# Kernel tuning notes

Measured on AMD Instinct MI355X. Metric: run time of the kernel, lower is better.

Reference implementation:

```python
import jax, jax.numpy as jnp
import numpy as np

B, LMAX, H, D = 128, 256, 16, 64
NEG_INF = -1e9  # finite mask value to keep padded softmax rows NaN-free


def _lengths():
    # deterministic varlen mix: 64 seqs of 128 tokens, 64 of 256 -> total 24576
    lens = np.array([128] * 64 + [256] * 64, dtype=np.int64)
    rng = np.random.default_rng(0)
    rng.shuffle(lens)
    return lens


def setup_inputs() -> dict:
    key = jax.random.key(0)
    lens = _lengths()
    cu = np.zeros(B + 1, dtype=np.int64)
    cu[1:] = np.cumsum(lens)
    T = int(cu[-1])  # 24576 packed tokens

    kq, kk, kv = jax.random.split(key, 3)
    q = jax.random.normal(kq, (T, H, D), dtype=jnp.float32)
    k = jax.random.normal(kk, (T, H, D), dtype=jnp.float32)
    v = jax.random.normal(kv, (T, H, D), dtype=jnp.float32)

    pos = np.arange(LMAX)[None, :]                      # [1, LMAX]
    mask = pos < lens[:, None]                          # [B, LMAX] valid-token mask
    gather_idx = np.where(mask, cu[:-1, None] + pos, 0).astype(np.int32)

    # packed token t -> flat padded index b*LMAX + (t - cu[b])
    b_of = np.repeat(np.arange(B), lens)
    inv_idx = (b_of * LMAX + (np.arange(T) - cu[b_of])).astype(np.int32)

    return {
        "q": q, "k": k, "v": v,
        "cu_seqlens_q": jnp.asarray(cu, dtype=jnp.int32),
        "cu_seqlens_k": jnp.asarray(cu, dtype=jnp.int32),
        "gather_idx": jnp.asarray(gather_idx),
        "mask": jnp.asarray(mask),
        "inv_idx": jnp.asarray(inv_idx),
        "max_seqlen_q": LMAX,
        "max_seqlen_k": LMAX,
    }


def reference(q, k, v, cu_seqlens_q, cu_seqlens_k, gather_idx, mask, inv_idx,
              max_seqlen_q, max_seqlen_k):
    # Pad packed [T,H,D] -> [B,L,H,D]; padded slots point at token 0 but are masked out.
    qp = q[gather_idx]  # [B, L, H, D]
    kp = k[gather_idx]
    vp = v[gather_idx]
    scale = 1.0 / jnp.sqrt(jnp.asarray(q.shape[-1], q.dtype))
    scores = jnp.einsum("bqhd,bkhd->bhqk", qp, kp) * scale  # [B, H, L, L]
    scores = jnp.where(mask[:, None, None, :], scores, NEG_INF)
    w = jax.nn.softmax(scores, axis=-1)
    out_p = jnp.einsum("bhqk,bkhd->bqhd", w, vp)            # [B, L, H, D]
    # Unpad back to packed layout [T, H, D]
    return out_p.reshape(-1, q.shape[1], q.shape[2])[inv_idx]
```

## Files before the change

kernel.cpp:

```cpp
#include <hip/hip_runtime.h>
#include <hip/hip_bf16.h>


using bf16x8 = __attribute__((ext_vector_type(8))) short;
using u16x8  = __attribute__((ext_vector_type(8))) unsigned short;
using u32x4  = __attribute__((ext_vector_type(4))) unsigned;
using f32x16 = __attribute__((ext_vector_type(16))) float;

#define MFMA32(a, b, c) __builtin_amdgcn_mfma_f32_32x32x16_bf16((a), (b), (c), 0, 0, 0)

constexpr int H  = 16;
constexpr int D  = 64;
constexpr int RS = H * D;
constexpr int NITEMS = 128 * 16;
constexpr float QSCALE = 0.125f * 1.44269504088896f;
constexpr float THR    = 11.5f;

__device__ inline unsigned short bfbits(float x) {
  return __builtin_bit_cast(unsigned short, __float2bfloat16(x));
}
__device__ inline float bff(unsigned short u) {
  unsigned v = ((unsigned)u) << 16;
  return __builtin_bit_cast(float, v);
}
__device__ inline unsigned pack2(float x, float y) {
  return (unsigned)bfbits(x) | ((unsigned)bfbits(y) << 16);
}

__global__ __launch_bounds__(512, 2)
void fa_persist13_kernel(const float* __restrict__ qg, const float* __restrict__ kg,
                         const float* __restrict__ vg, const int* __restrict__ cu,
                         float* __restrict__ outg, int* __restrict__ ctr) {
  __shared__ unsigned short kp4[4][64 * 64];
  __shared__ unsigned short vt4[4][64 * 64];
  __shared__ float lsc[8 * 32];
  __shared__ int item_s2[2];

  const int tid = (int)threadIdx.x, lane = tid & 63, w = tid >> 6;
  const int hi = lane >> 5, qj = lane & 31;
  const bool hib = (hi != 0);

  const int m7   = qj & 7;
  const int boff = (hi ^ m7) << 3;
  const int KA0  = qj * 64 + boff;
  const int KA1  = (32 + qj) * 64 + boff;

  const int k_key = tid >> 3, kd0 = (tid & 7) * 8;
  const int kidx  = k_key * 64 + ((((kd0 >> 3)) ^ (k_key & 7)) << 3);
  const int v_d = tid & 63, vk0 = (tid >> 6) * 8;
  const int vidx  = v_d * 64 + ((((vk0 >> 3)) ^ (v_d & 7)) << 3);

  if (tid == 0) item_s2[0] = atomicAdd(ctr, 1);
  int parity = 0;

  for (;;) {
    __syncthreads();
    const int item = item_s2[parity];
    if (item >= NITEMS) break;

    const int b = item >> 4, h = item & 15;
    const int t0 = cu[b];
    const int L  = cu[b + 1] - t0;
    const bool pair = (L == 128);
    if (pair && h >= 8) {
      if (tid == 0) item_s2[parity ^ 1] = atomicAdd(ctr, 1);
      parity ^= 1;
      continue;
    }

    const int myh    = pair ? ((w < 4) ? h : h + 8) : h;
    const int q_roff = pair ? (w & 3) * 32 : w * 32;
    const int hD  = h * D;
    const int h2D = (h + 8) * D;
    const int t_v1 = pair ? 0  : 64;  const int ho_v1 = pair ? h2D : hD;
    const int t_v2 = pair ? 64 : 128; const int ho_v2 = hD;
    const int t_v3 = pair ? 64 : 192; const int ho_v3 = pair ? h2D : hD;

    bf16x8 qh[4], ql[4];
    {
      const float* qrow = qg + (size_t)(t0 + q_roff + qj) * RS + (size_t)(myh * D);
#pragma unroll
      for (int ks = 0; ks < 4; ++ks) {
        const int d0 = ks * 16 + hi * 8;
        const float4 f0 = *reinterpret_cast<const float4*>(qrow + d0);
        const float4 f1 = *reinterpret_cast<const float4*>(qrow + d0 + 4);
        const float f[8] = {f0.x, f0.y, f0.z, f0.w, f1.x, f1.y, f1.z, f1.w};
#pragma unroll
        for (int j = 0; j < 8; ++j) {
          const float x = f[j] * QSCALE;
          const unsigned short hs = bfbits(x);
          qh[ks][j] = (short)hs;
          ql[ks][j] = (short)bfbits(x - bff(hs));
        }
      }
    }

    f32x16 acc0, acc1;
#pragma unroll
    for (int r = 0; r < 16; ++r) { acc0[r] = 0.f; acc1[r] = 0.f; }
    float m = -1e30f, lsum = 0.f;

    auto load_t = [&](float* kf, float* vf, int tokoff, int ho) {
      const float* kr = kg + (size_t)(t0 + tokoff + k_key) * RS + (size_t)(ho + kd0);
      const float4 f0 = *reinterpret_cast<const float4*>(kr);
      const float4 f1 = *reinterpret_cast<const float4*>(kr + 4);
      kf[0] = f0.x; kf[1] = f0.y; kf[2] = f0.z; kf[3] = f0.w;
      kf[4] = f1.x; kf[5] = f1.y; kf[6] = f1.z; kf[7] = f1.w;
      const float* vp = vg + (size_t)(t0 + tokoff + vk0) * RS + (size_t)(ho + v_d);
#pragma unroll
      for (int i = 0; i < 8; ++i) vf[i] = vp[(size_t)i * RS];
    };
    auto cvt_write = [&](const float* kf, const float* vf, int buf) {
      u16x8 kh8, v8;
#pragma unroll
      for (int i = 0; i < 8; ++i) {
        kh8[i] = bfbits(kf[i]);
        v8[i]  = bfbits(vf[i]);
      }
      *reinterpret_cast<u16x8*>(&kp4[buf][kidx]) = kh8;
      *reinterpret_cast<u16x8*>(&vt4[buf][vidx]) = v8;
    };

    auto mix4 = [&](unsigned a0, unsigned a1, unsigned a2, unsigned a3) -> u32x4 {
      const unsigned t02 = hib ? a0 : a2;
      const unsigned t13 = hib ? a1 : a3;
      const unsigned c02 = (unsigned)__shfl_xor((int)t02, 32);
      const unsigned c13 = (unsigned)__shfl_xor((int)t13, 32);
      u32x4 r;
      r[0] = hib ? c02 : a0;
      r[1] = hib ? c13 : a1;
      r[2] = hib ? a2 : c02;
      r[3] = hib ? a3 : c13;
      return r;
    };
    auto build_pa = [&](const float* x) -> bf16x8 {
      return __builtin_bit_cast(bf16x8,
          mix4(pack2(x[0], x[1]), pack2(x[2], x[3]),
               pack2(x[4], x[5]), pack2(x[6], x[7])));
    };

    auto compute = [&](const unsigned short* KH, const unsigned short* VT) {
      f32x16 sc0, sc1;
#pragma unroll
      for (int r = 0; r < 16; ++r) { sc0[r] = 0.f; sc1[r] = 0.f; }
#pragma unroll
      for (int ks = 0; ks < 4; ++ks) {
        const bf16x8 k0 = *reinterpret_cast<const bf16x8*>(&KH[KA0 ^ (ks << 4)]);
        sc0 = MFMA32(k0, qh[ks], sc0);
        sc0 = MFMA32(k0, ql[ks], sc0);
      }
#pragma unroll
      for (int ks = 0; ks < 4; ++ks) {
        const bf16x8 k1 = *reinterpret_cast<const bf16x8*>(&KH[KA1 ^ (ks << 4)]);
        sc1 = MFMA32(k1, qh[ks], sc1);
        sc1 = MFMA32(k1, ql[ks], sc1);
      }

      float mx[8];
#pragma unroll
      for (int i = 0; i < 8; ++i) mx[i] = fmaxf(sc0[i], sc0[i + 8]);
#pragma unroll
      for (int i = 0; i < 8; ++i) mx[i] = fmaxf(mx[i], fmaxf(sc1[i], sc1[i + 8]));
#pragma unroll
      for (int i = 0; i < 4; ++i) mx[i] = fmaxf(mx[i], mx[i + 4]);
      float tmax = fmaxf(fmaxf(mx[0], mx[1]), fmaxf(mx[2], mx[3]));
      tmax = fmaxf(tmax, __shfl_xor(tmax, 32));
      if (!__all(tmax <= m + THR)) {
        const float newm = fmaxf(m, tmax);
        const float corr = exp2f(m - newm);
        m = newm;
        lsum *= corr;
        if (hi == 0) lsc[w * 32 + qj] = corr;
        __builtin_amdgcn_wave_barrier();
#pragma unroll
        for (int r = 0; r < 16; ++r) {
          const float c = lsc[w * 32 + ((r & 3) + 8 * (r >> 2) + 4 * hi)];
          acc0[r] *= c; acc1[r] *= c;
        }
      }
      float s0 = 0.f, s1 = 0.f, s2 = 0.f, s3 = 0.f;
#pragma unroll
      for (int r = 0; r < 16; r += 4) {
        sc0[r]     = exp2f(sc0[r]     - m); s0 += sc0[r];
        sc0[r + 1] = exp2f(sc0[r + 1] - m); s1 += sc0[r + 1];
        sc0[r + 2] = exp2f(sc0[r + 2] - m); s2 += sc0[r + 2];
        sc0[r + 3] = exp2f(sc0[r + 3] - m); s3 += sc0[r + 3];
      }
#pragma unroll
      for (int r = 0; r < 16; r += 4) {
        sc1[r]     = exp2f(sc1[r]     - m); s0 += sc1[r];
        sc1[r + 1] = exp2f(sc1[r + 1] - m); s1 += sc1[r + 1];
        sc1[r + 2] = exp2f(sc1[r + 2] - m); s2 += sc1[r + 2];
        sc1[r + 3] = exp2f(sc1[r + 3] - m); s3 += sc1[r + 3];
      }
      lsum += (s0 + s1) + (s2 + s3);

#pragma unroll
      for (int ks2 = 0; ks2 < 4; ++ks2) {
        float px[8];
#pragma unroll
        for (int i = 0; i < 8; ++i)
          px[i] = (ks2 & 2) ? sc1[(ks2 & 1) * 8 + i] : sc0[(ks2 & 1) * 8 + i];
        const bf16x8 pah = build_pa(px);
        const bf16x8 v0 = *reinterpret_cast<const bf16x8*>(&VT[KA0 ^ (ks2 << 4)]);
        const bf16x8 v1 = *reinterpret_cast<const bf16x8*>(&VT[KA1 ^ (ks2 << 4)]);
        acc0 = MFMA32(pah, v0, acc0);
        acc1 = MFMA32(pah, v1, acc1);
      }
    };

#define LGKM_BARRIER()                                    \
    asm volatile("s_waitcnt lgkmcnt(0)" ::: "memory");    \
    __builtin_amdgcn_s_barrier();                         \
    asm volatile("" ::: "memory")

    float kfA[8], vfA[8], kfB[8], vfB[8];
    load_t(kfA, vfA, 0, hD);
    load_t(kfB, vfB, t_v1, ho_v1);
    cvt_write(kfA, vfA, 0);
    cvt_write(kfB, vfB, 1);
    LGKM_BARRIER();

    if (pair) {
      load_t(kfA, vfA, t_v2, ho_v2);
      load_t(kfB, vfB, t_v3, ho_v3);
      const int c1 = (w < 4) ? 0 : 1;
      compute(kp4[c1], vt4[c1]);
      cvt_write(kfA, vfA, 2);
      cvt_write(kfB, vfB, 3);
      LGKM_BARRIER();
      if (tid == 0) item_s2[parity ^ 1] = atomicAdd(ctr, 1);
      const int c2 = (w < 4) ? 2 : 3;
      compute(kp4[c2], vt4[c2]);
    } else {
      load_t(kfA, vfA, t_v2, ho_v2);
      compute(kp4[0], vt4[0]);
      cvt_write(kfA, vfA, 2);
      load_t(kfB, vfB, t_v3, ho_v3);
      compute(kp4[1], vt4[1]);
      cvt_write(kfB, vfB, 3);
      LGKM_BARRIER();
      if (tid == 0) item_s2[parity ^ 1] = atomicAdd(ctr, 1);
      compute(kp4[2], vt4[2]);
      compute(kp4[3], vt4[3]);
    }

    lsum += __shfl_xor(lsum, 32);
    if (hi == 0) lsc[w * 32 + qj] = 1.0f / lsum;
    __builtin_amdgcn_wave_barrier();
#pragma unroll
    for (int r = 0; r < 16; ++r) {
      const int row = (r & 3) + 8 * (r >> 2) + 4 * hi;
      const float li = lsc[w * 32 + row];
      float* op = outg + (size_t)(t0 + q_roff + row) * RS + (size_t)(myh * D) + qj;
      op[0]  = acc0[r] * li;
      op[32] = acc1[r] * li;
    }
    parity ^= 1;
  }
#undef LGKM_BARRIER
}

extern "C" void kernel_launch(void* const* d_in, const int* in_sizes, int n_in,
                              void* d_out, int out_size, void* d_ws, size_t ws_size,
                              hipStream_t stream) {
  (void)in_sizes; (void)n_in; (void)ws_size; (void)out_size;
  const float* q  = (const float*)d_in[0];
  const float* k  = (const float*)d_in[1];
  const float* v  = (const float*)d_in[2];
  const int*   cu = (const int*)d_in[3];
  float* out = (float*)d_out;
  int*   ctr = (int*)d_ws;

  hipMemsetAsync(ctr, 0, sizeof(int), stream);
  fa_persist13_kernel<<<dim3(512), dim3(512), 0, stream>>>(q, k, v, cu, out, ctr);
}
```

Before: 102.9 us.

## Prefetch next work item's first K/V tiles during current item's compute

Moves the atomic fetch of the next work item ahead of the barrier, then issues global loads for the next item's first two K/V tiles before the final compute phase of the current item. The aim is to hide the global-memory latency at the start of each persistent-loop iteration behind MFMA work. The cost is more live registers across the compute phase, which could cause spills or hurt the two-blocks-per-CU occupancy. The atomicAdd now sits before the lgkmcnt wait so its LDS write becomes visible after the barrier.

```diff
diff --git a/kernel.cpp b/kernel.cpp
--- a/kernel.cpp
+++ b/kernel.cpp
@@ -28,7 +28,7 @@
 }
 
 __global__ __launch_bounds__(512, 2)
-void fa_persist13_kernel(const float* __restrict__ qg, const float* __restrict__ kg,
+void fa_persist14_kernel(const float* __restrict__ qg, const float* __restrict__ kg,
                          const float* __restrict__ vg, const int* __restrict__ cu,
                          float* __restrict__ outg, int* __restrict__ ctr) {
   __shared__ unsigned short kp4[4][64 * 64];
@@ -50,8 +50,42 @@
   const int v_d = tid & 63, vk0 = (tid >> 6) * 8;
   const int vidx  = v_d * 64 + ((((vk0 >> 3)) ^ (v_d & 7)) << 3);
 
+  float kfA[8], vfA[8], kfB[8], vfB[8];
+  auto load_g = [&](float* kf, float* vf, int gt0, int tokoff, int ho) {
+    const float* kr = kg + (size_t)(gt0 + tokoff + k_key) * RS + (size_t)(ho + kd0);
+    const float4 f0 = *reinterpret_cast<const float4*>(kr);
+    const float4 f1 = *reinterpret_cast<const float4*>(kr + 4);
+    kf[0] = f0.x; kf[1] = f0.y; kf[2] = f0.z; kf[3] = f0.w;
+    kf[4] = f1.x; kf[5] = f1.y; kf[6] = f1.z; kf[7] = f1.w;
+    const float* vp = vg + (size_t)(gt0 + tokoff + vk0) * RS + (size_t)(ho + v_d);
+#pragma unroll
+    for (int i = 0; i < 8; ++i) vf[i] = vp[(size_t)i * RS];
+  };
+  auto cvt_write = [&](const float* kf, const float* vf, int buf) {
+    u16x8 kh8, v8;
+#pragma unroll
+    for (int i = 0; i < 8; ++i) {
+      kh8[i] = bfbits(kf[i]);
+      v8[i]  = bfbits(vf[i]);
+    }
+    *reinterpret_cast<u16x8*>(&kp4[buf][kidx]) = kh8;
+    *reinterpret_cast<u16x8*>(&vt4[buf][vidx]) = v8;
+  };
+  auto prefetch_item = [&](int nxt) -> bool {
+    if (nxt >= NITEMS) return false;
+    const int nb = nxt >> 4, nh = nxt & 15;
+    const int nt0 = cu[nb];
+    const bool npair = (cu[nb + 1] - nt0 == 128);
+    if (npair && nh >= 8) return false;
+    const int nhD = nh * D;
+    load_g(kfA, vfA, nt0, 0, nhD);
+    load_g(kfB, vfB, nt0, npair ? 0 : 64, npair ? (nh + 8) * D : nhD);
+    return true;
+  };
+
   if (tid == 0) item_s2[0] = atomicAdd(ctr, 1);
   int parity = 0;
+  bool have_pf = false;
 
   for (;;) {
     __syncthreads();
@@ -65,6 +99,7 @@
     if (pair && h >= 8) {
       if (tid == 0) item_s2[parity ^ 1] = atomicAdd(ctr, 1);
       parity ^= 1;
+      have_pf = false;
       continue;
     }
 
@@ -99,27 +134,6 @@
 #pragma unroll
     for (int r = 0; r < 16; ++r) { acc0[r] = 0.f; acc1[r] = 0.f; }
     float m = -1e30f, lsum = 0.f;
-
-    auto load_t = [&](float* kf, float* vf, int tokoff, int ho) {
-      const float* kr = kg + (size_t)(t0 + tokoff + k_key) * RS + (size_t)(ho + kd0);
-      const float4 f0 = *reinterpret_cast<const float4*>(kr);
-      const float4 f1 = *reinterpret_cast<const float4*>(kr + 4);
-      kf[0] = f0.x; kf[1] = f0.y; kf[2] = f0.z; kf[3] = f0.w;
-      kf[4] = f1.x; kf[5] = f1.y; kf[6] = f1.z; kf[7] = f1.w;
-      const float* vp = vg + (size_t)(t0 + tokoff + vk0) * RS + (size_t)(ho + v_d);
-#pragma unroll
-      for (int i = 0; i < 8; ++i) vf[i] = vp[(size_t)i * RS];
-    };
-    auto cvt_write = [&](const float* kf, const float* vf, int buf) {
-      u16x8 kh8, v8;
-#pragma unroll
-      for (int i = 0; i < 8; ++i) {
-        kh8[i] = bfbits(kf[i]);
-        v8[i]  = bfbits(vf[i]);
-      }
-      *reinterpret_cast<u16x8*>(&kp4[buf][kidx]) = kh8;
-      *reinterpret_cast<u16x8*>(&vt4[buf][vidx]) = v8;
-    };
 
     auto mix4 = [&](unsigned a0, unsigned a1, unsigned a2, unsigned a3) -> u32x4 {
       const unsigned t02 = hib ? a0 : a2;
@@ -214,33 +228,36 @@
     __builtin_amdgcn_s_barrier();                         \
     asm volatile("" ::: "memory")
 
-    float kfA[8], vfA[8], kfB[8], vfB[8];
-    load_t(kfA, vfA, 0, hD);
-    load_t(kfB, vfB, t_v1, ho_v1);
+    if (!have_pf) {
+      load_g(kfA, vfA, t0, 0, hD);
+      load_g(kfB, vfB, t0, t_v1, ho_v1);
+    }
     cvt_write(kfA, vfA, 0);
     cvt_write(kfB, vfB, 1);
     LGKM_BARRIER();
 
     if (pair) {
-      load_t(kfA, vfA, t_v2, ho_v2);
-      load_t(kfB, vfB, t_v3, ho_v3);
+      load_g(kfA, vfA, t0, t_v2, ho_v2);
+      load_g(kfB, vfB, t0, t_v3, ho_v3);
       const int c1 = (w < 4) ? 0 : 1;
       compute(kp4[c1], vt4[c1]);
       cvt_write(kfA, vfA, 2);
       cvt_write(kfB, vfB, 3);
+      if (tid == 0) item_s2[parity ^ 1] = atomicAdd(ctr, 1);
       LGKM_BARRIER();
-      if (tid == 0) item_s2[parity ^ 1] = atomicAdd(ctr, 1);
+      have_pf = prefetch_item(item_s2[parity ^ 1]);
       const int c2 = (w < 4) ? 2 : 3;
       compute(kp4[c2], vt4[c2]);
     } else {
-      load_t(kfA, vfA, t_v2, ho_v2);
+      load_g(kfA, vfA, t0, t_v2, ho_v2);
       compute(kp4[0], vt4[0]);
       cvt_write(kfA, vfA, 2);
-      load_t(kfB, vfB, t_v3, ho_v3);
+      load_g(kfB, vfB, t0, t_v3, ho_v3);
       compute(kp4[1], vt4[1]);
       cvt_write(kfB, vfB, 3);
+      if (tid == 0) item_s2[parity ^ 1] = atomicAdd(ctr, 1);
       LGKM_BARRIER();
-      if (tid == 0) item_s2[parity ^ 1] = atomicAdd(ctr, 1);
+      have_pf = prefetch_item(item_s2[parity ^ 1]);
       compute(kp4[2], vt4[2]);
       compute(kp4[3], vt4[3]);
     }
@@ -273,5 +290,5 @@
   int*   ctr = (int*)d_ws;
 
   hipMemsetAsync(ctr, 0, sizeof(int), stream);
-  fa_persist13_kernel<<<dim3(512), dim3(512), 0, stream>>>(q, k, v, cu, out, ctr);
-}
+  fa_persist14_kernel<<<dim3(512), dim3(512), 0, stream>>>(q, k, v, cu, out, ctr);
+}
```

Result: no change. 104.9 us (+2.0%).
